# Optimization experiments

Measured on AMD Instinct MI355X. Metric: run time of the kernel, lower is better.

## Reference

```python
import jax, jax.numpy as jnp
import numpy as np

D_MODEL = 512
D_ATTN = 512

def setup_inputs() -> dict:
    key = jax.random.key(0)
    kx, kq, kk, kv = jax.random.split(key, 4)
    x = jax.random.normal(kx, (8, 2048, D_MODEL), dtype=jnp.float32)
    s = 1.0 / np.sqrt(D_MODEL)
    Wq = jax.random.normal(kq, (D_ATTN, D_MODEL), dtype=jnp.float32) * s
    Wk = jax.random.normal(kk, (D_ATTN, D_MODEL), dtype=jnp.float32) * s
    Wv = jax.random.normal(kv, (D_MODEL, D_MODEL), dtype=jnp.float32) * s
    return {"x": x, "Wq": Wq, "Wk": Wk, "Wv": Wv}

def reference(x, Wq, Wk, Wv):
    # x: [B, S, D]; Linear(bias=False): y = x @ W.T
    q = jnp.einsum('bsd,ad->bsa', x, Wq)  # [B,S,Da]
    k = jnp.einsum('bsd,ad->bsa', x, Wk)  # [B,S,Da]
    v = jnp.einsum('bsd,ed->bse', x, Wv)  # [B,S,Dv]
    scale = 1.0 / jnp.sqrt(jnp.asarray(q.shape[-1], dtype=q.dtype))
    scores = jnp.einsum('bqa,bka->bqk', q, k) * scale  # [B,S,S]
    p = jax.nn.softmax(scores, axis=-1)
    return jnp.einsum('bqk,bke->bqe', p, v)
```

## Files before the change

### kernel.cpp

```cpp
#include <hip/hip_runtime.h>


typedef __bf16 bf16x8 __attribute__((ext_vector_type(8)));
typedef __bf16 bf16x4 __attribute__((ext_vector_type(4)));
typedef float  f32x4  __attribute__((ext_vector_type(4)));

constexpr int SEQ = 2048;
constexpr int DM  = 512;
constexpr int NB  = 8;
constexpr int GS  = NB * SEQ;
constexpr int NT2 = SEQ / 32;

__device__ __forceinline__ void gl16(const void* g, void* l) {
  __builtin_amdgcn_global_load_lds((const __attribute__((address_space(1))) void*)g,
                                   (__attribute__((address_space(3))) void*)l, 16, 0, 0);
}

__device__ __forceinline__ f32x4 mfma16(bf16x8 a, bf16x8 b, f32x4 c) {
  return __builtin_amdgcn_mfma_f32_16x16x32_bf16(a, b, c, 0, 0, 0);
}

__global__ void convert_kernel(const float* __restrict__ x,
                               const float* __restrict__ wq,
                               const float* __restrict__ wk,
                               const float* __restrict__ wv,
                               __bf16* __restrict__ xb,
                               __bf16* __restrict__ wqb,
                               __bf16* __restrict__ wkb,
                               __bf16* __restrict__ wvb) {
  const int NX4 = (GS * DM) / 4;
  const int NW4 = (DM * DM) / 4;
  const int stride = gridDim.x * blockDim.x;
  const int tid = blockIdx.x * blockDim.x + threadIdx.x;
  for (int i = tid; i < NX4; i += stride) {
    float4 v = ((const float4*)x)[i];
    bf16x4 o = { (__bf16)v.x, (__bf16)v.y, (__bf16)v.z, (__bf16)v.w };
    ((bf16x4*)xb)[i] = o;
  }
  for (int i = tid; i < NW4; i += stride) {
    float4 v = ((const float4*)wq)[i];
    bf16x4 o = { (__bf16)v.x, (__bf16)v.y, (__bf16)v.z, (__bf16)v.w };
    ((bf16x4*)wqb)[i] = o;
  }
  for (int i = tid; i < NW4; i += stride) {
    float4 v = ((const float4*)wk)[i];
    bf16x4 o = { (__bf16)v.x, (__bf16)v.y, (__bf16)v.z, (__bf16)v.w };
    ((bf16x4*)wkb)[i] = o;
  }
  for (int i = tid; i < NW4; i += stride) {
    float4 v = ((const float4*)wv)[i];
    bf16x4 o = { (__bf16)v.x, (__bf16)v.y, (__bf16)v.z, (__bf16)v.w };
    ((bf16x4*)wvb)[i] = o;
  }
}

__global__ __launch_bounds__(256, 2) void gemm_nt_kernel(
    const __bf16* __restrict__ A, const __bf16* __restrict__ Bm,
    __bf16* __restrict__ C, int N) {
  __shared__ __bf16 As[128 * 32];
  __shared__ __bf16 Bs[128 * 32];
  const int t = threadIdx.x;
  const int w = t >> 6, l = t & 63;
  const int l15 = l & 15, lg = l >> 4;
  const int m0 = blockIdx.x * 128, n0 = blockIdx.y * 128;
  const int wr = w >> 1, wc = w & 1;

  f32x4 acc[4][4] = {};
  const char* Ab = (const char*)A + (size_t)m0 * (DM * 2);
  const char* Bb = (const char*)Bm + (size_t)n0 * (DM * 2);

  for (int k0 = 0; k0 < DM; k0 += 32) {
#pragma unroll
    for (int i = 0; i < 2; ++i) {
      const int f = (i * 256 + t) * 16;
      const int row = f >> 6, c = f & 63;
      gl16(Ab + (size_t)row * (DM * 2) + k0 * 2 + c, (char*)As + f);
      gl16(Bb + (size_t)row * (DM * 2) + k0 * 2 + c, (char*)Bs + f);
    }
    __syncthreads();
    bf16x8 af[4], bfr[4];
#pragma unroll
    for (int mi = 0; mi < 4; ++mi)
      af[mi] = *(const bf16x8*)((const char*)As + (wr * 64 + mi * 16 + l15) * 64 + lg * 16);
#pragma unroll
    for (int ni = 0; ni < 4; ++ni)
      bfr[ni] = *(const bf16x8*)((const char*)Bs + (wc * 64 + ni * 16 + l15) * 64 + lg * 16);
#pragma unroll
    for (int mi = 0; mi < 4; ++mi)
#pragma unroll
      for (int ni = 0; ni < 4; ++ni)
        acc[mi][ni] = mfma16(af[mi], bfr[ni], acc[mi][ni]);
    __syncthreads();
  }
#pragma unroll
  for (int mi = 0; mi < 4; ++mi)
#pragma unroll
    for (int ni = 0; ni < 4; ++ni)
#pragma unroll
      for (int r = 0; r < 4; ++r) {
        const int row = m0 + wr * 64 + mi * 16 + lg * 4 + r;
        const int col = n0 + wc * 64 + ni * 16 + l15;
        C[(size_t)row * N + col] = (__bf16)acc[mi][ni][r];
      }
}

__global__ __launch_bounds__(512, 2) void attn_kernel(
    const __bf16* __restrict__ QK, const __bf16* __restrict__ Vt,
    float* __restrict__ Out) {
  __shared__ __bf16 Ks[2][32 * 512];
  __shared__ __bf16 Vs[2][512 * 32];
  __shared__ float  Ss[64 * 36];
  __shared__ __bf16 Ps[64 * 32];
  __shared__ float  m_s[64], l_s[64], corr_s[64];
  __shared__ int    flags_s[8];

  const int t = threadIdx.x;
  const int w = t >> 6, l = t & 63;
  const int l15 = l & 15, lg = l >> 4;
  const int b = blockIdx.x & 7;
  const int q0 = (blockIdx.x >> 3) * 64;
  const int qi = w >> 1, kj = w & 1;

  int ksrc[4], vsrc[4], ldst[4];
#pragma unroll
  for (int i = 0; i < 4; ++i) {
    const int f = (i * 512 + t) * 16;
    ldst[i] = f;
    const int krow = f >> 10, kc = f & 1023;
    ksrc[i] = krow * 2048 + (kc ^ ((krow & 7) << 4));
    const int e = f >> 6, c2 = f & 63;
    vsrc[i] = e * (GS * 2) + (c2 ^ ((e & 3) << 4));
  }

  const char* Kb = (const char*)QK + (size_t)b * SEQ * 2048 + 1024;
  const char* Vb = (const char*)Vt + (size_t)b * SEQ * 2;

  bf16x8 qf[16];
  {
    const char* Qb = (const char*)QK +
        (size_t)(b * SEQ + q0 + qi * 16 + l15) * 2048 + lg * 16;
#pragma unroll
    for (int ks = 0; ks < 16; ++ks)
      qf[ks] = *(const bf16x8*)(Qb + ks * 64);
  }

  f32x4 o[4][4] = {};
  if (t < 64) { m_s[t] = -__builtin_inff(); l_s[t] = 0.f; }

#pragma unroll
  for (int i = 0; i < 4; ++i) gl16(Kb + ksrc[i], (char*)&Ks[0][0] + ldst[i]);
#pragma unroll
  for (int i = 0; i < 4; ++i) gl16(Vb + vsrc[i], (char*)&Vs[0][0] + ldst[i]);

  const float SCL = 0.0637639022f;

  for (int it = 0; it < NT2; ++it) {
    const int cur = it & 1;

    asm volatile("s_waitcnt vmcnt(0) lgkmcnt(0)" ::: "memory");
    __builtin_amdgcn_s_barrier();

    {
      const int kvn = (it + 1 < NT2 ? it + 1 : 0) * 32;
      char* kdst = (char*)&Ks[cur ^ 1][0];
      char* vdst = (char*)&Vs[cur ^ 1][0];
#pragma unroll
      for (int i = 0; i < 4; ++i) gl16(Kb + (size_t)kvn * 2048 + ksrc[i], kdst + ldst[i]);
#pragma unroll
      for (int i = 0; i < 4; ++i) gl16(Vb + (size_t)kvn * 2 + vsrc[i], vdst + ldst[i]);
    }

    {
      f32x4 s0 = {}, s1 = {};
      const int krow = kj * 16 + l15;
      const char* KsR = (const char*)&Ks[cur][0] + krow * 1024;
      const int ksw = (krow & 7) << 4;
      __builtin_amdgcn_s_setprio(1);
#pragma unroll
      for (int ks = 0; ks < 8; ++ks) {
        bf16x8 kf0 = *(const bf16x8*)(KsR + ((ks * 64 + lg * 16) ^ ksw));
        bf16x8 kf1 = *(const bf16x8*)(KsR + (((ks + 8) * 64 + lg * 16) ^ ksw));
        s0 = mfma16(qf[ks], kf0, s0);
        s1 = mfma16(qf[ks + 8], kf1, s1);
      }
      __builtin_amdgcn_s_setprio(0);
      s0 = s0 + s1;
#pragma unroll
      for (int r = 0; r < 4; ++r)
        Ss[(qi * 16 + lg * 4 + r) * 36 + kj * 16 + l15] = s0[r] * SCL;
    }
    asm volatile("s_waitcnt lgkmcnt(0)" ::: "memory");
    __builtin_amdgcn_s_barrier();

    {
      const int row = t >> 3, c8 = t & 7;
      float4 v0 = *(const float4*)&Ss[row * 36 + c8 * 4];
      float tmax = fmaxf(fmaxf(v0.x, v0.y), fmaxf(v0.z, v0.w));
      tmax = fmaxf(tmax, __shfl_xor(tmax, 1));
      tmax = fmaxf(tmax, __shfl_xor(tmax, 2));
      tmax = fmaxf(tmax, __shfl_xor(tmax, 4));
      const float mold = m_s[row];
      const float mnew = fmaxf(mold, tmax);
      const float corr = exp2f(mold - mnew);
      const float p0 = exp2f(v0.x - mnew), p1 = exp2f(v0.y - mnew);
      const float p2 = exp2f(v0.z - mnew), p3 = exp2f(v0.w - mnew);
      float rsum = (p0 + p1) + (p2 + p3);
      rsum += __shfl_xor(rsum, 1);
      rsum += __shfl_xor(rsum, 2);
      rsum += __shfl_xor(rsum, 4);
      if (c8 == 0) { m_s[row] = mnew; l_s[row] = l_s[row] * corr + rsum; corr_s[row] = corr; }
      const int allskip = __all(corr == 1.0f);
      if (l == 0) flags_s[w] = allskip;
      bf16x4 pb = { (__bf16)p0, (__bf16)p1, (__bf16)p2, (__bf16)p3 };
      *(bf16x4*)((char*)Ps + row * 64 + (((c8 >> 1) * 16) ^ ((row & 3) << 4)) +
                 (c8 & 1) * 8) = pb;
    }
    asm volatile("s_waitcnt lgkmcnt(0)" ::: "memory");
    __builtin_amdgcn_s_barrier();

    {
      int fl = 1;
#pragma unroll
      for (int i = 0; i < 8; ++i) fl &= flags_s[i];
      if (!fl) {
#pragma unroll
        for (int mi = 0; mi < 4; ++mi) {
          float cr[4];
#pragma unroll
          for (int r = 0; r < 4; ++r) cr[r] = corr_s[mi * 16 + lg * 4 + r];
#pragma unroll
          for (int ni = 0; ni < 4; ++ni)
#pragma unroll
            for (int r = 0; r < 4; ++r) o[mi][ni][r] *= cr[r];
        }
      }
      bf16x8 pf[4];
#pragma unroll
      for (int mi = 0; mi < 4; ++mi) {
        const int prow = mi * 16 + l15;
        pf[mi] = *(const bf16x8*)((const char*)Ps + prow * 64 +
                                  ((lg * 16) ^ ((prow & 3) << 4)));
      }
      __builtin_amdgcn_s_setprio(1);
#pragma unroll
      for (int ni = 0; ni < 4; ++ni) {
        const int er = w * 64 + ni * 16 + l15;
        bf16x8 vf = *(const bf16x8*)((const char*)&Vs[cur][0] + er * 64 +
                                     ((lg * 16) ^ ((er & 3) << 4)));
#pragma unroll
        for (int mi = 0; mi < 4; ++mi)
          o[mi][ni] = mfma16(pf[mi], vf, o[mi][ni]);
      }
      __builtin_amdgcn_s_setprio(0);
    }
  }

#pragma unroll
  for (int mi = 0; mi < 4; ++mi) {
    float rl[4];
#pragma unroll
    for (int r = 0; r < 4; ++r) rl[r] = 1.0f / l_s[mi * 16 + lg * 4 + r];
#pragma unroll
    for (int ni = 0; ni < 4; ++ni)
#pragma unroll
      for (int r = 0; r < 4; ++r) {
        const int row = q0 + mi * 16 + lg * 4 + r;
        const int col = w * 64 + ni * 16 + l15;
        Out[((size_t)b * SEQ + row) * DM + col] = o[mi][ni][r] * rl[r];
      }
  }
}

extern "C" void kernel_launch(void* const* d_in, const int* in_sizes, int n_in,
                              void* d_out, int out_size, void* d_ws, size_t ws_size,
                              hipStream_t stream) {
  const float* x  = (const float*)d_in[0];
  const float* wq = (const float*)d_in[1];
  const float* wk = (const float*)d_in[2];
  const float* wv = (const float*)d_in[3];
  float* out = (float*)d_out;
  char* ws = (char*)d_ws;

  __bf16* xb   = (__bf16*)(ws);
  __bf16* wqkb = (__bf16*)(ws + 16777216);
  __bf16* wvb  = (__bf16*)(ws + 17825792);
  __bf16* qk   = (__bf16*)(ws + 18350080);
  __bf16* vt   = (__bf16*)(ws + 51904512);

  convert_kernel<<<2048, 256, 0, stream>>>(x, wq, wk, wv,
                                           xb, wqkb, wqkb + 262144, wvb);
  gemm_nt_kernel<<<dim3(GS / 128, 1024 / 128), 256, 0, stream>>>(xb, wqkb, qk, 1024);
  gemm_nt_kernel<<<dim3(DM / 128, GS / 128), 256, 0, stream>>>(wvb, xb, vt, GS);
  attn_kernel<<<256, 512, 0, stream>>>(qk, vt, out);
}
```

Measured before the change: 289.6 us.

## Restructure attention into per-wave register softmax with split-KV halves and merge

Rewrites the attention kernel so each pair of waves owns 16 query rows and each wave takes half of every 64-key tile. Softmax state stays in registers and reductions use shuffles, which removes the shared score/P buffers and several barriers per iteration. Each wave accumulates the full 512-wide output (32 accumulators) and the two halves are merged through LDS at the end. The softmax scale is folded into Wq during conversion. In exchange, KV tiles are single-buffered with loads staged between barriers, and the large accumulator set raises register pressure.

```diff
diff --git a/kernel.cpp b/kernel.cpp
--- a/kernel.cpp
+++ b/kernel.cpp
@@ -9,7 +9,7 @@
 constexpr int DM  = 512;
 constexpr int NB  = 8;
 constexpr int GS  = NB * SEQ;
-constexpr int NT2 = SEQ / 32;
+constexpr int NT  = SEQ / 64;
 
 __device__ __forceinline__ void gl16(const void* g, void* l) {
   __builtin_amdgcn_global_load_lds((const __attribute__((address_space(1))) void*)g,
@@ -30,6 +30,7 @@
                                __bf16* __restrict__ wvb) {
   const int NX4 = (GS * DM) / 4;
   const int NW4 = (DM * DM) / 4;
+  const float SCL = 0.0637639022f;
   const int stride = gridDim.x * blockDim.x;
   const int tid = blockIdx.x * blockDim.x + threadIdx.x;
   for (int i = tid; i < NX4; i += stride) {
@@ -39,7 +40,8 @@
   }
   for (int i = tid; i < NW4; i += stride) {
     float4 v = ((const float4*)wq)[i];
-    bf16x4 o = { (__bf16)v.x, (__bf16)v.y, (__bf16)v.z, (__bf16)v.w };
+    bf16x4 o = { (__bf16)(v.x * SCL), (__bf16)(v.y * SCL),
+                 (__bf16)(v.z * SCL), (__bf16)(v.w * SCL) };
     ((bf16x4*)wqb)[i] = o;
   }
   for (int i = tid; i < NW4; i += stride) {
@@ -107,167 +109,187 @@
 __global__ __launch_bounds__(512, 2) void attn_kernel(
     const __bf16* __restrict__ QK, const __bf16* __restrict__ Vt,
     float* __restrict__ Out) {
-  __shared__ __bf16 Ks[2][32 * 512];
-  __shared__ __bf16 Vs[2][512 * 32];
-  __shared__ float  Ss[64 * 36];
-  __shared__ __bf16 Ps[64 * 32];
-  __shared__ float  m_s[64], l_s[64], corr_s[64];
-  __shared__ int    flags_s[8];
+  __shared__ __align__(16) __bf16 Ks[64 * 512];
+  __shared__ __align__(16) __bf16 Vs[512 * 64];
 
   const int t = threadIdx.x;
   const int w = t >> 6, l = t & 63;
   const int l15 = l & 15, lg = l >> 4;
   const int b = blockIdx.x & 7;
   const int q0 = (blockIdx.x >> 3) * 64;
-  const int qi = w >> 1, kj = w & 1;
-
-  int ksrc[4], vsrc[4], ldst[4];
-#pragma unroll
-  for (int i = 0; i < 4; ++i) {
-    const int f = (i * 512 + t) * 16;
-    ldst[i] = f;
-    const int krow = f >> 10, kc = f & 1023;
-    ksrc[i] = krow * 2048 + (kc ^ ((krow & 7) << 4));
-    const int e = f >> 6, c2 = f & 63;
-    vsrc[i] = e * (GS * 2) + (c2 ^ ((e & 3) << 4));
-  }
-
-  const char* Kb = (const char*)QK + (size_t)b * SEQ * 2048 + 1024;
-  const char* Vb = (const char*)Vt + (size_t)b * SEQ * 2;
+  const int pair = w >> 1;
+  const int wv = w & 1;
+
+  const char* QKc = (const char*)QK;
+  const char* Vtc = (const char*)Vt;
+  char* KsB = (char*)Ks;
+  char* VsB = (char*)Vs;
+
+  const int kcol = (l * 16) ^ ((w & 3) << 5);
+  const size_t kbase = (size_t)(b * SEQ) * 2048 + 1024;
+  const int vrow = t >> 3;
+  const int vcol = ((t & 7) * 16) ^ ((vrow & 7) << 4);
+  const size_t vbase = (size_t)(b * SEQ) * 2;
+
+  const int r0 = wv * 32 + ((l15 & 12) << 1) + (l15 & 3);
+  const int Xk = ((l15 & 3) << 1) | ((l15 >> 2) & 1);
+  const int kb0 = r0 * 1024, kb1 = kb0 + 4096;
+  const int voff = (((lg + wv * 4) ^ (l15 & 7)) << 4) + l15 * 128;
 
   bf16x8 qf[16];
   {
-    const char* Qb = (const char*)QK +
-        (size_t)(b * SEQ + q0 + qi * 16 + l15) * 2048 + lg * 16;
+    const char* Qp = QKc + (size_t)(b * SEQ + q0 + pair * 16 + l15) * 2048 + lg * 16;
 #pragma unroll
     for (int ks = 0; ks < 16; ++ks)
-      qf[ks] = *(const bf16x8*)(Qb + ks * 64);
-  }
-
-  f32x4 o[4][4] = {};
-  if (t < 64) { m_s[t] = -__builtin_inff(); l_s[t] = 0.f; }
-
-#pragma unroll
-  for (int i = 0; i < 4; ++i) gl16(Kb + ksrc[i], (char*)&Ks[0][0] + ldst[i]);
-#pragma unroll
-  for (int i = 0; i < 4; ++i) gl16(Vb + vsrc[i], (char*)&Vs[0][0] + ldst[i]);
-
-  const float SCL = 0.0637639022f;
-
-  for (int it = 0; it < NT2; ++it) {
-    const int cur = it & 1;
-
-    asm volatile("s_waitcnt vmcnt(0) lgkmcnt(0)" ::: "memory");
+      qf[ks] = *(const bf16x8*)(Qp + ks * 64);
+  }
+
+#pragma unroll
+  for (int i = 0; i < 8; ++i)
+    gl16(QKc + kbase + (size_t)(i * 8 + w) * 2048 + (kcol ^ ((i & 1) << 4)),
+         KsB + (i * 512 + t) * 16);
+#pragma unroll
+  for (int i = 0; i < 8; ++i)
+    gl16(Vtc + vbase + (size_t)(i * 64 + vrow) * (GS * 2) + vcol,
+         VsB + (i * 512 + t) * 16);
+
+  asm volatile("s_waitcnt vmcnt(16)" ::: "memory");
+  __builtin_amdgcn_sched_barrier(0);
+
+  f32x4 o[32] = {};
+  float m_run = -__builtin_inff(), l_run = 0.f;
+
+  for (int it = 0; it < NT; ++it) {
+    const int kvn = (it + 1 < NT ? it + 1 : 0) * 64;
+
+    asm volatile("s_waitcnt vmcnt(8)" ::: "memory");
+    __builtin_amdgcn_sched_barrier(0);
     __builtin_amdgcn_s_barrier();
 
-    {
-      const int kvn = (it + 1 < NT2 ? it + 1 : 0) * 32;
-      char* kdst = (char*)&Ks[cur ^ 1][0];
-      char* vdst = (char*)&Vs[cur ^ 1][0];
-#pragma unroll
-      for (int i = 0; i < 4; ++i) gl16(Kb + (size_t)kvn * 2048 + ksrc[i], kdst + ldst[i]);
-#pragma unroll
-      for (int i = 0; i < 4; ++i) gl16(Vb + (size_t)kvn * 2 + vsrc[i], vdst + ldst[i]);
+    f32x4 s0 = {}, s1 = {};
+    __builtin_amdgcn_s_setprio(1);
+#pragma unroll
+    for (int ks = 0; ks < 16; ++ks) {
+      const int c0 = ((ks * 4 + lg) ^ Xk) << 4;
+      bf16x8 kf0 = *(const bf16x8*)(KsB + kb0 + c0);
+      bf16x8 kf1 = *(const bf16x8*)(KsB + kb1 + c0);
+      s0 = mfma16(kf0, qf[ks], s0);
+      s1 = mfma16(kf1, qf[ks], s1);
     }
-
-    {
-      f32x4 s0 = {}, s1 = {};
-      const int krow = kj * 16 + l15;
-      const char* KsR = (const char*)&Ks[cur][0] + krow * 1024;
-      const int ksw = (krow & 7) << 4;
-      __builtin_amdgcn_s_setprio(1);
-#pragma unroll
-      for (int ks = 0; ks < 8; ++ks) {
-        bf16x8 kf0 = *(const bf16x8*)(KsR + ((ks * 64 + lg * 16) ^ ksw));
-        bf16x8 kf1 = *(const bf16x8*)(KsR + (((ks + 8) * 64 + lg * 16) ^ ksw));
-        s0 = mfma16(qf[ks], kf0, s0);
-        s1 = mfma16(qf[ks + 8], kf1, s1);
-      }
-      __builtin_amdgcn_s_setprio(0);
-      s0 = s0 + s1;
+    __builtin_amdgcn_s_setprio(0);
+    __builtin_amdgcn_s_barrier();
+
+#pragma unroll
+    for (int i = 0; i < 8; ++i)
+      gl16(QKc + kbase + (size_t)(kvn + i * 8 + w) * 2048 + (kcol ^ ((i & 1) << 4)),
+           KsB + (i * 512 + t) * 16);
+
+    float p0 = s0[0], p1 = s0[1], p2 = s0[2], p3 = s0[3];
+    float p4 = s1[0], p5 = s1[1], p6 = s1[2], p7 = s1[3];
+    float tmax = fmaxf(fmaxf(fmaxf(p0, p1), fmaxf(p2, p3)),
+                       fmaxf(fmaxf(p4, p5), fmaxf(p6, p7)));
+    tmax = fmaxf(tmax, __shfl_xor(tmax, 16));
+    tmax = fmaxf(tmax, __shfl_xor(tmax, 32));
+    const float mnew = fmaxf(m_run, tmax);
+    const float corr = exp2f(m_run - mnew);
+    p0 = exp2f(p0 - mnew); p1 = exp2f(p1 - mnew);
+    p2 = exp2f(p2 - mnew); p3 = exp2f(p3 - mnew);
+    p4 = exp2f(p4 - mnew); p5 = exp2f(p5 - mnew);
+    p6 = exp2f(p6 - mnew); p7 = exp2f(p7 - mnew);
+    float rsum = ((p0 + p1) + (p2 + p3)) + ((p4 + p5) + (p6 + p7));
+    rsum += __shfl_xor(rsum, 16);
+    rsum += __shfl_xor(rsum, 32);
+    l_run = l_run * corr + rsum;
+    m_run = mnew;
+    const bf16x8 pa = { (__bf16)p0, (__bf16)p1, (__bf16)p2, (__bf16)p3,
+                        (__bf16)p4, (__bf16)p5, (__bf16)p6, (__bf16)p7 };
+
+    if (!__all(corr == 1.0f)) {
+      float cr[4];
+#pragma unroll
+      for (int r = 0; r < 4; ++r) cr[r] = __shfl(corr, lg * 4 + r);
+#pragma unroll
+      for (int f = 0; f < 32; ++f)
+#pragma unroll
+        for (int r = 0; r < 4; ++r) o[f][r] *= cr[r];
+    }
+
+    asm volatile("s_waitcnt vmcnt(8)" ::: "memory");
+    __builtin_amdgcn_sched_barrier(0);
+    __builtin_amdgcn_s_barrier();
+
+    __builtin_amdgcn_s_setprio(1);
+#pragma unroll
+    for (int f = 0; f < 32; ++f) {
+      bf16x8 vf = *(const bf16x8*)(VsB + f * 2048 + voff);
+      o[f] = mfma16(pa, vf, o[f]);
+    }
+    __builtin_amdgcn_s_setprio(0);
+    __builtin_amdgcn_s_barrier();
+
+#pragma unroll
+    for (int i = 0; i < 8; ++i)
+      gl16(Vtc + vbase + (size_t)kvn * 2 + (size_t)(i * 64 + vrow) * (GS * 2) + vcol,
+           VsB + (i * 512 + t) * 16);
+  }
+
+  asm volatile("s_waitcnt vmcnt(0)" ::: "memory");
+  __builtin_amdgcn_sched_barrier(0);
+  __builtin_amdgcn_s_barrier();
+
+  float* Sx = (float*)KsB;
+  if (l < 16) {
+    Sx[(pair * 2 + wv) * 32 + l15] = m_run;
+    Sx[(pair * 2 + wv) * 32 + 16 + l15] = l_run;
+  }
+  __builtin_amdgcn_s_barrier();
+  const float mP = Sx[(pair * 2 + (wv ^ 1)) * 32 + l15];
+  const float lP = Sx[(pair * 2 + (wv ^ 1)) * 32 + 16 + l15];
+  const float mst = fmaxf(m_run, mP);
+  const float lst = l_run * exp2f(m_run - mst) + lP * exp2f(mP - mst);
+  const float sc = exp2f(m_run - mst) / lst;
+  __builtin_amdgcn_s_barrier();
+
+  float cs[4];
+#pragma unroll
+  for (int r = 0; r < 4; ++r) cs[r] = __shfl(sc, lg * 4 + r);
+#pragma unroll
+  for (int f = 0; f < 32; ++f)
+#pragma unroll
+    for (int r = 0; r < 4; ++r) o[f][r] *= cs[r];
+
+  float* R0 = (float*)KsB + pair * 4096;
+  float* R1 = (float*)VsB + pair * 4096;
+  if (wv == 1) {
+#pragma unroll
+    for (int f = 0; f < 16; ++f)
 #pragma unroll
       for (int r = 0; r < 4; ++r)
-        Ss[(qi * 16 + lg * 4 + r) * 36 + kj * 16 + l15] = s0[r] * SCL;
-    }
-    asm volatile("s_waitcnt lgkmcnt(0)" ::: "memory");
-    __builtin_amdgcn_s_barrier();
-
-    {
-      const int row = t >> 3, c8 = t & 7;
-      float4 v0 = *(const float4*)&Ss[row * 36 + c8 * 4];
-      float tmax = fmaxf(fmaxf(v0.x, v0.y), fmaxf(v0.z, v0.w));
-      tmax = fmaxf(tmax, __shfl_xor(tmax, 1));
-      tmax = fmaxf(tmax, __shfl_xor(tmax, 2));
-      tmax = fmaxf(tmax, __shfl_xor(tmax, 4));
-      const float mold = m_s[row];
-      const float mnew = fmaxf(mold, tmax);
-      const float corr = exp2f(mold - mnew);
-      const float p0 = exp2f(v0.x - mnew), p1 = exp2f(v0.y - mnew);
-      const float p2 = exp2f(v0.z - mnew), p3 = exp2f(v0.w - mnew);
-      float rsum = (p0 + p1) + (p2 + p3);
-      rsum += __shfl_xor(rsum, 1);
-      rsum += __shfl_xor(rsum, 2);
-      rsum += __shfl_xor(rsum, 4);
-      if (c8 == 0) { m_s[row] = mnew; l_s[row] = l_s[row] * corr + rsum; corr_s[row] = corr; }
-      const int allskip = __all(corr == 1.0f);
-      if (l == 0) flags_s[w] = allskip;
-      bf16x4 pb = { (__bf16)p0, (__bf16)p1, (__bf16)p2, (__bf16)p3 };
-      *(bf16x4*)((char*)Ps + row * 64 + (((c8 >> 1) * 16) ^ ((row & 3) << 4)) +
-                 (c8 & 1) * 8) = pb;
-    }
-    asm volatile("s_waitcnt lgkmcnt(0)" ::: "memory");
-    __builtin_amdgcn_s_barrier();
-
-    {
-      int fl = 1;
-#pragma unroll
-      for (int i = 0; i < 8; ++i) fl &= flags_s[i];
-      if (!fl) {
-#pragma unroll
-        for (int mi = 0; mi < 4; ++mi) {
-          float cr[4];
-#pragma unroll
-          for (int r = 0; r < 4; ++r) cr[r] = corr_s[mi * 16 + lg * 4 + r];
-#pragma unroll
-          for (int ni = 0; ni < 4; ++ni)
-#pragma unroll
-            for (int r = 0; r < 4; ++r) o[mi][ni][r] *= cr[r];
-        }
-      }
-      bf16x8 pf[4];
-#pragma unroll
-      for (int mi = 0; mi < 4; ++mi) {
-        const int prow = mi * 16 + l15;
-        pf[mi] = *(const bf16x8*)((const char*)Ps + prow * 64 +
-                                  ((lg * 16) ^ ((prow & 3) << 4)));
-      }
-      __builtin_amdgcn_s_setprio(1);
-#pragma unroll
-      for (int ni = 0; ni < 4; ++ni) {
-        const int er = w * 64 + ni * 16 + l15;
-        bf16x8 vf = *(const bf16x8*)((const char*)&Vs[cur][0] + er * 64 +
-                                     ((lg * 16) ^ ((er & 3) << 4)));
-#pragma unroll
-        for (int mi = 0; mi < 4; ++mi)
-          o[mi][ni] = mfma16(pf[mi], vf, o[mi][ni]);
-      }
-      __builtin_amdgcn_s_setprio(0);
-    }
-  }
-
-#pragma unroll
-  for (int mi = 0; mi < 4; ++mi) {
-    float rl[4];
-#pragma unroll
-    for (int r = 0; r < 4; ++r) rl[r] = 1.0f / l_s[mi * 16 + lg * 4 + r];
-#pragma unroll
-    for (int ni = 0; ni < 4; ++ni)
-#pragma unroll
-      for (int r = 0; r < 4; ++r) {
-        const int row = q0 + mi * 16 + lg * 4 + r;
-        const int col = w * 64 + ni * 16 + l15;
-        Out[((size_t)b * SEQ + row) * DM + col] = o[mi][ni][r] * rl[r];
-      }
+        R0[(lg * 4 + r) * 256 + f * 16 + l15] = o[f][r];
+  } else {
+#pragma unroll
+    for (int f = 16; f < 32; ++f)
+#pragma unroll
+      for (int r = 0; r < 4; ++r)
+        R1[(lg * 4 + r) * 256 + (f - 16) * 16 + l15] = o[f][r];
+  }
+  __builtin_amdgcn_s_barrier();
+
+  float* Op = Out + ((size_t)b * SEQ + q0 + pair * 16) * DM;
+  if (wv == 0) {
+#pragma unroll
+    for (int f = 0; f < 16; ++f)
+#pragma unroll
+      for (int r = 0; r < 4; ++r)
+        Op[(lg * 4 + r) * DM + f * 16 + l15] =
+            o[f][r] + R0[(lg * 4 + r) * 256 + f * 16 + l15];
+  } else {
+#pragma unroll
+    for (int f = 16; f < 32; ++f)
+#pragma unroll
+      for (int r = 0; r < 4; ++r)
+        Op[(lg * 4 + r) * DM + f * 16 + l15] =
+            o[f][r] + R1[(lg * 4 + r) * 256 + (f - 16) * 16 + l15];
   }
 }
 
```

New measurement: 632.8 us. +118.5%, slower.
